# Optimization experiments

Measured on AMD Instinct MI355X. Metric: run time of the kernel, lower is better.

The kernel has to match this reference:

```python
import jax, jax.numpy as jnp
import numpy as np

N_NODES = 100000
N_EDGES = 1600000
IN_FEATS = 128
HIDDEN = 64
OUT_FEATS = 64
N_LABELS = 8


def setup_inputs() -> dict:
    key = jax.random.key(0)
    ks = jax.random.split(key, 10)
    glorot = lambda k, fi, fo: jax.random.normal(k, (fi, fo), jnp.float32) * jnp.sqrt(2.0 / (fi + fo))
    return {
        "features": jax.random.normal(ks[0], (N_NODES, IN_FEATS), jnp.float32),
        "edge_src": jax.random.randint(ks[1], (N_EDGES,), 0, N_NODES, jnp.int32),
        "edge_dst": jax.random.randint(ks[2], (N_EDGES,), 0, N_NODES, jnp.int32),
        "edge_types": jax.random.randint(ks[3], (N_EDGES,), 0, 4, jnp.int32),
        "W1": glorot(ks[4], IN_FEATS, HIDDEN),
        "b1": jnp.zeros((HIDDEN,), jnp.float32),
        "W2": glorot(ks[5], HIDDEN, OUT_FEATS),
        "b2": jnp.zeros((OUT_FEATS,), jnp.float32),
        "Wp": glorot(ks[6], OUT_FEATS, N_LABELS),
        "bp": jnp.zeros((N_LABELS,), jnp.float32),
    }


def _degree_norms(edge_src, edge_dst, n_nodes):
    ones = jnp.ones(edge_src.shape[0], jnp.float32)
    deg_out = jax.ops.segment_sum(ones, edge_src, num_segments=n_nodes)
    deg_in = jax.ops.segment_sum(ones, edge_dst, num_segments=n_nodes)
    # DGL clamps degrees to min 1 before pow(-0.5)
    norm_src = jnp.maximum(deg_out, 1.0) ** -0.5  # [N]
    norm_dst = jnp.maximum(deg_in, 1.0) ** -0.5   # [N]
    return norm_src, norm_dst


def _graph_conv(x, W, b, edge_src, edge_dst, norm_src, norm_dst, n_nodes):
    # norm='both': scale src, dense transform first (mult_first), aggregate, scale dst
    h = (x * norm_src[:, None]) @ W            # [N, out]
    msg = h[edge_src]                          # [E, out] gather
    agg = jax.ops.segment_sum(msg, edge_dst, num_segments=n_nodes)  # [N, out] scatter-add
    return agg * norm_dst[:, None] + b


def reference(features, edge_src, edge_dst, edge_types, W1, b1, W2, b2, Wp, bp):
    n_nodes = features.shape[0]
    norm_src, norm_dst = _degree_norms(edge_src, edge_dst, n_nodes)
    x = jax.nn.relu(_graph_conv(features, W1, b1, edge_src, edge_dst, norm_src, norm_dst, n_nodes))
    # dropout is identity in eval mode
    x = jax.nn.relu(_graph_conv(x, W2, b2, edge_src, edge_dst, norm_src, norm_dst, n_nodes))
    logits = x @ Wp + bp                       # [N, n_labels]
    return jax.nn.softmax(logits, axis=1)
```

## Files before the change

### kernel.cpp

```cpp
#include <hip/hip_runtime.h>
#include <hip/hip_fp16.h>
#include <math.h>


#define NODES   100000
#define INF     128
#define HID     64
#define NLAB    8

#define SB      512
#define NSB     ((NODES + SB - 1) / SB)
#define NHALF   ((NODES + 255) / 256)
#define CAP1    9000
#define SCAP    9000
#define CAP2    4600
#define PCHUNK  8192
#define PEPT    (PCHUNK / 256)
#define SRCMASK 0x1FFFF
#define GSTRIDE 16

#define WCVT_ELEMS (64 * (INF + 8) + 64 * (HID + 8))
#define WCVT_WGS   ((WCVT_ELEMS + 255) / 256)

union H8 { int4 i4; __half2 h2[4]; };

typedef _Float16 half8 __attribute__((ext_vector_type(8)));
typedef float floatx4 __attribute__((ext_vector_type(4)));


__global__ void build1_kernel(const int* __restrict__ src, const int* __restrict__ dst,
                              int* __restrict__ gcur_d, int* __restrict__ gcur_s,
                              int* __restrict__ dreg, unsigned short* __restrict__ sreg,
                              int E, int partWGs,
                              const float* __restrict__ W1, const float* __restrict__ W2,
                              _Float16* __restrict__ wt1, _Float16* __restrict__ wt2) {
    __shared__ int hd[NSB], hs[NSB], bd[NSB], bs[NSB];
    const int tid = threadIdx.x;

    if (blockIdx.x >= partWGs) {
        const int N1 = 64 * (INF + 8);
        const int N2 = 64 * (HID + 8);
        int i = (blockIdx.x - partWGs) * 256 + tid;
        if (i < N1) {
            int n = i / (INF + 8), k = i % (INF + 8);
            wt1[i] = (k < INF) ? (_Float16)W1[k * 64 + n] : (_Float16)0.f;
        } else if (i < N1 + N2) {
            int j = i - N1;
            int n = j / (HID + 8), k = j % (HID + 8);
            wt2[j] = (k < HID) ? (_Float16)W2[k * 64 + n] : (_Float16)0.f;
        }
        return;
    }

    const int e0 = blockIdx.x * PCHUNK;

    for (int i = tid; i < NSB; i += 256) { hd[i] = 0; hs[i] = 0; }
    __syncthreads();

    int es[PEPT], ed[PEPT];
#pragma unroll
    for (int i = 0; i < PEPT; ++i) {
        int e = e0 + tid + i * 256;
        if (e < E) {
            es[i] = src[e]; ed[i] = dst[e];
            atomicAdd(&hd[ed[i] >> 9], 1);
            atomicAdd(&hs[es[i] >> 9], 1);
        } else es[i] = -1;
    }
    __syncthreads();

    for (int b = tid; b < NSB; b += 256) {
        int c = hd[b]; bd[b] = c ? atomicAdd(&gcur_d[b * GSTRIDE], c) : 0;
        c = hs[b];     bs[b] = c ? atomicAdd(&gcur_s[b * GSTRIDE], c) : 0;
    }
    __syncthreads();
    for (int b = tid; b < NSB; b += 256) { hd[b] = 0; hs[b] = 0; }
    __syncthreads();

#pragma unroll
    for (int i = 0; i < PEPT; ++i) {
        if (es[i] >= 0) {
            int s = es[i], d = ed[i];
            int kb = d >> 9;
            int pos = bd[kb] + atomicAdd(&hd[kb], 1);
            if (pos < CAP1) dreg[(size_t)kb * CAP1 + pos] = ((d & (SB - 1)) << 17) | s;
            int ks = s >> 9;
            int ps = bs[ks] + atomicAdd(&hs[ks], 1);
            if (ps < SCAP) sreg[(size_t)ks * SCAP + ps] = (unsigned short)(s & (SB - 1));
        }
    }
}


__global__ void shist_kernel(const unsigned short* __restrict__ sreg,
                             const int* __restrict__ gcur_s,
                             float* __restrict__ norm_s, int Nn) {
    __shared__ int hist[SB];
    const int tid = threadIdx.x;
    const int sb = blockIdx.x;
    for (int i = tid; i < SB; i += 256) hist[i] = 0;
    __syncthreads();
    const int cnt = min(gcur_s[sb * GSTRIDE], SCAP);
    const unsigned short* base = sreg + (size_t)sb * SCAP;
    for (int i = tid; i < cnt; i += 256) atomicAdd(&hist[base[i]], 1);
    __syncthreads();
    for (int t = tid; t < SB; t += 256) {
        int node = sb * SB + t;
        if (node < Nn) norm_s[node] = rsqrtf(fmaxf((float)hist[t], 1.0f));
    }
}


__global__ void build2_kernel(const int* __restrict__ dreg, const int* __restrict__ gcur_d,
                              int* __restrict__ csr, int* __restrict__ starts,
                              int* __restrict__ ends, float* __restrict__ norm_d,
                              const float* __restrict__ Xv, const float* __restrict__ norm,
                              const _Float16* __restrict__ Wt, __half* __restrict__ Hh,
                              int Nn) {
    __shared__ union SMem {
        struct CS { int hist[256]; int excl[256]; int cur[256]; int tot; int sorted[CAP2]; } c;
        _Float16 w[64 * (INF + 8)];
    } sm;
    const int tid = threadIdx.x;

    if (blockIdx.x < NHALF) {
        const int j = blockIdx.x;
        const int sb = j >> 1, half = j & 1;
        const int cnt = min(gcur_d[sb * GSTRIDE], CAP1);
        const int* reg = dreg + (size_t)sb * CAP1;

        sm.c.hist[tid] = 0;
        __syncthreads();

        for (int i = tid; i < cnt; i += 256) {
            int pe = reg[i];
            if (((pe >> 25) & 1) == half) atomicAdd(&sm.c.hist[(pe >> 17) & 255], 1);
        }
        __syncthreads();

        sm.c.excl[tid] = sm.c.hist[tid];
        __syncthreads();
        for (int off = 1; off < 256; off <<= 1) {
            int v = (tid >= off) ? sm.c.excl[tid - off] : 0;
            __syncthreads();
            sm.c.excl[tid] += v;
            __syncthreads();
        }
        int deg_n = sm.c.hist[tid];
        int st = sm.c.excl[tid] - deg_n;
        if (tid == 255) sm.c.tot = min(sm.c.excl[255], CAP2);
        int node = j * 256 + tid;
        if (node < Nn) {
            int gs = j * CAP2 + st;
            int dcl = min(deg_n, max(CAP2 - st, 0));
            starts[node] = gs;
            ends[node]   = gs + dcl;
            norm_d[node] = rsqrtf(fmaxf((float)deg_n, 1.0f));
        }
        sm.c.cur[tid] = st;
        __syncthreads();

        for (int i = tid; i < cnt; i += 256) {
            int pe = reg[i];
            if (((pe >> 25) & 1) == half) {
                int pos = atomicAdd(&sm.c.cur[(pe >> 17) & 255], 1);
                if (pos < CAP2) sm.c.sorted[pos] = pe & SRCMASK;
            }
        }
        __syncthreads();

        const int tot = sm.c.tot;
        for (int i = tid; i < tot; i += 256) csr[(size_t)j * CAP2 + i] = sm.c.sorted[i];
        return;
    }

    constexpr int K = INF;
    constexpr int KP = K + 8;
    const int bid = blockIdx.x - NHALF;

    constexpr int NI4 = 64 * KP * 2 / 16;
    for (int i = tid; i < NI4; i += 256)
        ((int4*)sm.w)[i] = ((const int4*)Wt)[i];
    __syncthreads();

    const int w = tid >> 6, lane = tid & 63;
    const int m16 = lane & 15, quad = lane >> 4;
    const int rowA = bid * 64 + w * 16 + m16;
    const int rowC = (rowA < Nn) ? rowA : (Nn - 1);

    floatx4 acc0 = {0.f, 0.f, 0.f, 0.f};
    floatx4 acc1 = acc0, acc2 = acc0, acc3 = acc0;

#pragma unroll
    for (int c = 0; c < K / 32; ++c) {
        const int k0 = c * 32 + quad * 8;
        const float* xrow = Xv + (size_t)rowC * K;
        float4 xa = *(const float4*)(xrow + k0);
        float4 xb = *(const float4*)(xrow + k0 + 4);
        half8 a;
        a[0] = (_Float16)xa.x; a[1] = (_Float16)xa.y;
        a[2] = (_Float16)xa.z; a[3] = (_Float16)xa.w;
        a[4] = (_Float16)xb.x; a[5] = (_Float16)xb.y;
        a[6] = (_Float16)xb.z; a[7] = (_Float16)xb.w;
        half8 b0 = *(const half8*)&sm.w[(0 * 16 + m16) * KP + k0];
        half8 b1 = *(const half8*)&sm.w[(1 * 16 + m16) * KP + k0];
        half8 b2 = *(const half8*)&sm.w[(2 * 16 + m16) * KP + k0];
        half8 b3 = *(const half8*)&sm.w[(3 * 16 + m16) * KP + k0];
        acc0 = __builtin_amdgcn_mfma_f32_16x16x32_f16(a, b0, acc0, 0, 0, 0);
        acc1 = __builtin_amdgcn_mfma_f32_16x16x32_f16(a, b1, acc1, 0, 0, 0);
        acc2 = __builtin_amdgcn_mfma_f32_16x16x32_f16(a, b2, acc2, 0, 0, 0);
        acc3 = __builtin_amdgcn_mfma_f32_16x16x32_f16(a, b3, acc3, 0, 0, 0);
    }

    const int rbase = bid * 64 + w * 16 + quad * 4;
    floatx4 accs[4] = {acc0, acc1, acc2, acc3};
#pragma unroll
    for (int i = 0; i < 4; ++i) {
        int grow = rbase + i;
        if (grow < Nn) {
            float nm = norm[grow];
            __half* o = Hh + (size_t)grow * 64 + m16;
#pragma unroll
            for (int t = 0; t < 4; ++t)
                o[16 * t] = (__half)(accs[t][i] * nm);
        }
    }
}


template <int K, bool IN16>
__global__ void gemm_mfma_kernel(const void* __restrict__ Xv, const float* __restrict__ norm,
                                 const _Float16* __restrict__ Wt, __half* __restrict__ Hh,
                                 int M) {
    constexpr int KP = K + 8;
    __shared__ _Float16 sWt[64 * KP];

    const int tid = threadIdx.x;
    constexpr int NI4 = 64 * KP * 2 / 16;
    for (int i = tid; i < NI4; i += 256)
        ((int4*)sWt)[i] = ((const int4*)Wt)[i];
    __syncthreads();

    const int w = tid >> 6, lane = tid & 63;
    const int m16 = lane & 15, quad = lane >> 4;
    const int rowA = blockIdx.x * 64 + w * 16 + m16;
    const int rowC = (rowA < M) ? rowA : (M - 1);

    floatx4 acc0 = {0.f, 0.f, 0.f, 0.f};
    floatx4 acc1 = acc0, acc2 = acc0, acc3 = acc0;

#pragma unroll
    for (int c = 0; c < K / 32; ++c) {
        const int k0 = c * 32 + quad * 8;
        half8 a;
        if constexpr (IN16) {
            const _Float16* xrow = (const _Float16*)Xv + (size_t)rowC * K;
            a = *(const half8*)(xrow + k0);
        } else {
            const float* xrow = (const float*)Xv + (size_t)rowC * K;
            float4 xa = *(const float4*)(xrow + k0);
            float4 xb = *(const float4*)(xrow + k0 + 4);
            a[0] = (_Float16)xa.x; a[1] = (_Float16)xa.y;
            a[2] = (_Float16)xa.z; a[3] = (_Float16)xa.w;
            a[4] = (_Float16)xb.x; a[5] = (_Float16)xb.y;
            a[6] = (_Float16)xb.z; a[7] = (_Float16)xb.w;
        }
        half8 b0 = *(const half8*)&sWt[(0 * 16 + m16) * KP + k0];
        half8 b1 = *(const half8*)&sWt[(1 * 16 + m16) * KP + k0];
        half8 b2 = *(const half8*)&sWt[(2 * 16 + m16) * KP + k0];
        half8 b3 = *(const half8*)&sWt[(3 * 16 + m16) * KP + k0];
        acc0 = __builtin_amdgcn_mfma_f32_16x16x32_f16(a, b0, acc0, 0, 0, 0);
        acc1 = __builtin_amdgcn_mfma_f32_16x16x32_f16(a, b1, acc1, 0, 0, 0);
        acc2 = __builtin_amdgcn_mfma_f32_16x16x32_f16(a, b2, acc2, 0, 0, 0);
        acc3 = __builtin_amdgcn_mfma_f32_16x16x32_f16(a, b3, acc3, 0, 0, 0);
    }

    const int rbase = blockIdx.x * 64 + w * 16 + quad * 4;
    floatx4 accs[4] = {acc0, acc1, acc2, acc3};
#pragma unroll
    for (int i = 0; i < 4; ++i) {
        int grow = rbase + i;
        if (grow < M) {
            float nm = norm[grow];
            __half* o = Hh + (size_t)grow * 64 + m16;
#pragma unroll
            for (int t = 0; t < 4; ++t)
                o[16 * t] = (__half)(accs[t][i] * nm);
        }
    }
}


template <bool PROJ>
__global__ void gather_kernel(const int* __restrict__ starts, const int* __restrict__ ends,
                              const int* __restrict__ csr, const __half* __restrict__ Hh,
                              const float* __restrict__ nd, const float* __restrict__ b,
                              __half* __restrict__ Xh, const float* __restrict__ Wp,
                              const float* __restrict__ bp, float* __restrict__ out,
                              int Nn) {
    __shared__ float sW[NLAB * 65];
    __shared__ float sb_[NLAB];
    const int tid = threadIdx.x;

    if constexpr (PROJ) {
        for (int i = tid; i < 64 * NLAB; i += 256) {
            int k = i >> 3, l = i & 7;
            sW[l * 65 + k] = Wp[i];
        }
        if (tid < NLAB) sb_[tid] = bp[tid];
        __syncthreads();
    }

    const int lane = tid & 63;
    const int half32 = (lane >> 5) & 1;
    const int l32 = lane & 31;
    const int g = l32 >> 3;
    const int c = lane & 7;

    int node = blockIdx.x * 8 + ((tid >> 6) << 1) + half32;
    const bool valid = node < Nn;
    const int nodeC = valid ? node : (Nn - 1);

    const int start = starts[nodeC];
    const int deg   = ends[nodeC] - start;
    const int dmax  = max(deg, __shfl_xor(deg, 32, 64));

    float acc[8] = {0.f, 0.f, 0.f, 0.f, 0.f, 0.f, 0.f, 0.f};

    for (int base = 0; base < dmax; base += 32) {
        int off = base + l32;
        int pe = (off < deg) ? csr[start + off] : 0;
        int ec  = min(deg - base, 32);
        int ecm = min(dmax - base, 32);
        int nkp = (ecm + 7) >> 3;

        for (int k = 0; k < nkp; ++k) {
            int j0 = g + 8 * k;
            int j1 = j0 + 4;
            int s0 = __shfl(pe, (lane & 32) + j0, 64);
            int s1 = __shfl(pe, (lane & 32) + j1, 64);
            H8 v0, v1;
            if (j0 < ec) v0.i4 = ((const int4*)(Hh + (size_t)s0 * 64))[c];
            else         v0.i4 = make_int4(0, 0, 0, 0);
            if (j1 < ec) v1.i4 = ((const int4*)(Hh + (size_t)s1 * 64))[c];
            else         v1.i4 = make_int4(0, 0, 0, 0);
#pragma unroll
            for (int t = 0; t < 4; ++t) {
                __half2 s = __hadd2(v0.h2[t], v1.h2[t]);
                float2 f = __half22float2(s);
                acc[2 * t]     += f.x;
                acc[2 * t + 1] += f.y;
            }
        }
    }

#pragma unroll
    for (int m = 8; m <= 16; m <<= 1) {
#pragma unroll
        for (int k = 0; k < 8; ++k)
            acc[k] += __shfl_xor(acc[k], m, 64);
    }

    if constexpr (!PROJ) {
        if (g == 0 && valid) {
            float nm = nd[node];
            float4 b0 = ((const float4*)b)[2 * c];
            float4 b1 = ((const float4*)b)[2 * c + 1];
            H8 o;
            o.h2[0] = __floats2half2_rn(fmaxf(fmaf(acc[0], nm, b0.x), 0.f),
                                        fmaxf(fmaf(acc[1], nm, b0.y), 0.f));
            o.h2[1] = __floats2half2_rn(fmaxf(fmaf(acc[2], nm, b0.z), 0.f),
                                        fmaxf(fmaf(acc[3], nm, b0.w), 0.f));
            o.h2[2] = __floats2half2_rn(fmaxf(fmaf(acc[4], nm, b1.x), 0.f),
                                        fmaxf(fmaf(acc[5], nm, b1.y), 0.f));
            o.h2[3] = __floats2half2_rn(fmaxf(fmaf(acc[6], nm, b1.z), 0.f),
                                        fmaxf(fmaf(acc[7], nm, b1.w), 0.f));
            ((int4*)(Xh + (size_t)node * 64))[c] = o.i4;
        }
    } else {
        float nm = nd[nodeC];
        float4 b0 = ((const float4*)b)[2 * c];
        float4 b1 = ((const float4*)b)[2 * c + 1];
        float xv[8];
        xv[0] = fmaxf(fmaf(acc[0], nm, b0.x), 0.f);
        xv[1] = fmaxf(fmaf(acc[1], nm, b0.y), 0.f);
        xv[2] = fmaxf(fmaf(acc[2], nm, b0.z), 0.f);
        xv[3] = fmaxf(fmaf(acc[3], nm, b0.w), 0.f);
        xv[4] = fmaxf(fmaf(acc[4], nm, b1.x), 0.f);
        xv[5] = fmaxf(fmaf(acc[5], nm, b1.y), 0.f);
        xv[6] = fmaxf(fmaf(acc[6], nm, b1.z), 0.f);
        xv[7] = fmaxf(fmaf(acc[7], nm, b1.w), 0.f);

        const int l0 = 2 * g, l1 = l0 + 1;
        float p0 = 0.f, p1 = 0.f;
#pragma unroll
        for (int j = 0; j < 8; ++j) {
            p0 = fmaf(xv[j], sW[l0 * 65 + 8 * c + j], p0);
            p1 = fmaf(xv[j], sW[l1 * 65 + 8 * c + j], p1);
        }
        p0 += __shfl_xor(p0, 1, 64); p1 += __shfl_xor(p1, 1, 64);
        p0 += __shfl_xor(p0, 2, 64); p1 += __shfl_xor(p1, 2, 64);
        p0 += __shfl_xor(p0, 4, 64); p1 += __shfl_xor(p1, 4, 64);
        p0 += sb_[l0];
        p1 += sb_[l1];
        float mx = fmaxf(p0, p1);
        mx = fmaxf(mx, __shfl_xor(mx, 8, 64));
        mx = fmaxf(mx, __shfl_xor(mx, 16, 64));
        float e0 = __expf(p0 - mx), e1 = __expf(p1 - mx);
        float s2 = e0 + e1;
        s2 += __shfl_xor(s2, 8, 64);
        s2 += __shfl_xor(s2, 16, 64);
        float inv = 1.0f / s2;
        if (c == 0 && valid) {
            float2 o = {e0 * inv, e1 * inv};
            *(float2*)(out + (size_t)node * NLAB + l0) = o;
        }
    }
}


extern "C" void kernel_launch(void* const* d_in, const int* in_sizes, int n_in,
                              void* d_out, int out_size, void* d_ws, size_t ws_size,
                              hipStream_t stream) {
    const float* features = (const float*)d_in[0];
    const int*   edge_src = (const int*)d_in[1];
    const int*   edge_dst = (const int*)d_in[2];
    const float* W1 = (const float*)d_in[4];
    const float* b1 = (const float*)d_in[5];
    const float* W2 = (const float*)d_in[6];
    const float* b2 = (const float*)d_in[7];
    const float* Wp = (const float*)d_in[8];
    const float* bp = (const float*)d_in[9];
    float* out = (float*)d_out;

    const int N = NODES;
    const int E = in_sizes[1];

    char* p = (char*)d_ws;
    int*   csr    = (int*)p;            p += sizeof(int) * (size_t)NHALF * CAP2;
    int*   starts = (int*)p;            p += sizeof(int) * N;
    int*   ends   = (int*)p;            p += sizeof(int) * N;
    float* norm_s = (float*)p;          p += sizeof(float) * N;
    float* norm_d = (float*)p;          p += sizeof(float) * N;
    int*   gcur_d = (int*)p;            p += sizeof(int) * NSB * GSTRIDE;
    int*   gcur_s = (int*)p;            p += sizeof(int) * NSB * GSTRIDE;
    p = (char*)(((size_t)p + 255) & ~(size_t)255);
    _Float16* wt1 = (_Float16*)p;       p += sizeof(_Float16) * 64 * (INF + 8);
    _Float16* wt2 = (_Float16*)p;       p += sizeof(_Float16) * 64 * (HID + 8);
    p = (char*)(((size_t)p + 255) & ~(size_t)255);
    __half* h     = (__half*)p;         p += sizeof(__half) * (size_t)N * 64;
    p = (char*)(((size_t)p + 255) & ~(size_t)255);
    __half* x     = (__half*)p;         p += sizeof(__half) * (size_t)N * 64;
    int*            dreg = (int*)x;
    unsigned short* sreg = (unsigned short*)((char*)x + sizeof(int) * (size_t)NSB * CAP1);

    hipMemsetAsync(gcur_d, 0, sizeof(int) * 2 * NSB * GSTRIDE, stream);

    const int partWGs = (E + PCHUNK - 1) / PCHUNK;
    build1_kernel<<<partWGs + WCVT_WGS, 256, 0, stream>>>(edge_src, edge_dst,
                                                          gcur_d, gcur_s, dreg, sreg,
                                                          E, partWGs, W1, W2, wt1, wt2);
    shist_kernel<<<NSB, 256, 0, stream>>>(sreg, gcur_s, norm_s, N);
    build2_kernel<<<NHALF + (N + 63) / 64, 256, 0, stream>>>(dreg, gcur_d, csr, starts,
                                                             ends, norm_d,
                                                             features, norm_s, wt1, h, N);

    gather_kernel<false><<<(N + 7) / 8, 256, 0, stream>>>(starts, ends, csr, h, norm_d,
                                                          b1, x, nullptr, nullptr,
                                                          nullptr, N);

    gemm_mfma_kernel<HID, true><<<(N + 63) / 64, 256, 0, stream>>>(x, norm_s, wt2, h, N);
    gather_kernel<true><<<(N + 7) / 8, 256, 0, stream>>>(starts, ends, csr, h, norm_d,
                                                         b2, nullptr, Wp, bp, out, N);
}
```

Measured before the change: 249.7 us.

## Bucket destination edges per 256-node half-block and use fma_mix accumulation

Destination edges are now partitioned directly into 256-node buckets instead of 512-node buckets. Each build2 workgroup therefore reads only its own edges, with no half-filter that discards about half of what it loads. The block prefix scan now uses wavefront shuffles instead of a multi-barrier shared-memory scan. The gather inner loop converts fp16 to fp32 and adds in one step with v_fma_mix instructions. The costs are double the number of global bucket counters and atomics in build1, and inline assembly tied to the target ISA.

```diff
diff --git a/kernel.cpp b/kernel.cpp
--- a/kernel.cpp
+++ b/kernel.cpp
@@ -11,9 +11,8 @@
 #define SB      512
 #define NSB     ((NODES + SB - 1) / SB)
 #define NHALF   ((NODES + 255) / 256)
-#define CAP1    9000
 #define SCAP    9000
-#define CAP2    4600
+#define CAPH    4600
 #define PCHUNK  8192
 #define PEPT    (PCHUNK / 256)
 #define SRCMASK 0x1FFFF
@@ -22,10 +21,17 @@
 #define WCVT_ELEMS (64 * (INF + 8) + 64 * (HID + 8))
 #define WCVT_WGS   ((WCVT_ELEMS + 255) / 256)
 
-union H8 { int4 i4; __half2 h2[4]; };
+union H8 { int4 i4; __half2 h2[4]; unsigned int u[4]; };
+union H2U { __half2 h; unsigned int u; };
 
 typedef _Float16 half8 __attribute__((ext_vector_type(8)));
 typedef float floatx4 __attribute__((ext_vector_type(4)));
+
+__device__ __forceinline__ void fma_mix2(float& a0, float& a1, unsigned int h2) {
+    asm("v_fma_mix_f32 %0, %2, 1.0, %0 op_sel_hi:[1,0,0]\n\t"
+        "v_fma_mix_f32 %1, %2, 1.0, %1 op_sel:[1,0,0] op_sel_hi:[1,0,0]"
+        : "+v"(a0), "+v"(a1) : "v"(h2));
+}
 
 
 __global__ void build1_kernel(const int* __restrict__ src, const int* __restrict__ dst,
@@ -34,7 +40,7 @@
                               int E, int partWGs,
                               const float* __restrict__ W1, const float* __restrict__ W2,
                               _Float16* __restrict__ wt1, _Float16* __restrict__ wt2) {
-    __shared__ int hd[NSB], hs[NSB], bd[NSB], bs[NSB];
+    __shared__ int hd[NHALF], bd[NHALF], hs[NSB], bs[NSB];
     const int tid = threadIdx.x;
 
     if (blockIdx.x >= partWGs) {
@@ -54,7 +60,8 @@
 
     const int e0 = blockIdx.x * PCHUNK;
 
-    for (int i = tid; i < NSB; i += 256) { hd[i] = 0; hs[i] = 0; }
+    for (int i = tid; i < NHALF; i += 256) { hd[i] = 0; }
+    for (int i = tid; i < NSB; i += 256) { hs[i] = 0; }
     __syncthreads();
 
     int es[PEPT], ed[PEPT];
@@ -63,27 +70,30 @@
         int e = e0 + tid + i * 256;
         if (e < E) {
             es[i] = src[e]; ed[i] = dst[e];
-            atomicAdd(&hd[ed[i] >> 9], 1);
+            atomicAdd(&hd[ed[i] >> 8], 1);
             atomicAdd(&hs[es[i] >> 9], 1);
         } else es[i] = -1;
     }
     __syncthreads();
 
+    for (int b = tid; b < NHALF; b += 256) {
+        int c = hd[b]; bd[b] = c ? atomicAdd(&gcur_d[b * GSTRIDE], c) : 0;
+    }
     for (int b = tid; b < NSB; b += 256) {
-        int c = hd[b]; bd[b] = c ? atomicAdd(&gcur_d[b * GSTRIDE], c) : 0;
-        c = hs[b];     bs[b] = c ? atomicAdd(&gcur_s[b * GSTRIDE], c) : 0;
-    }
-    __syncthreads();
-    for (int b = tid; b < NSB; b += 256) { hd[b] = 0; hs[b] = 0; }
+        int c = hs[b]; bs[b] = c ? atomicAdd(&gcur_s[b * GSTRIDE], c) : 0;
+    }
+    __syncthreads();
+    for (int b = tid; b < NHALF; b += 256) hd[b] = 0;
+    for (int b = tid; b < NSB; b += 256) hs[b] = 0;
     __syncthreads();
 
 #pragma unroll
     for (int i = 0; i < PEPT; ++i) {
         if (es[i] >= 0) {
             int s = es[i], d = ed[i];
-            int kb = d >> 9;
+            int kb = d >> 8;
             int pos = bd[kb] + atomicAdd(&hd[kb], 1);
-            if (pos < CAP1) dreg[(size_t)kb * CAP1 + pos] = ((d & (SB - 1)) << 17) | s;
+            if (pos < CAPH) dreg[(size_t)kb * CAPH + pos] = ((d & 255) << 17) | s;
             int ks = s >> 9;
             int ps = bs[ks] + atomicAdd(&hs[ks], 1);
             if (ps < SCAP) sreg[(size_t)ks * SCAP + ps] = (unsigned short)(s & (SB - 1));
@@ -118,41 +128,42 @@
                               const _Float16* __restrict__ Wt, __half* __restrict__ Hh,
                               int Nn) {
     __shared__ union SMem {
-        struct CS { int hist[256]; int excl[256]; int cur[256]; int tot; int sorted[CAP2]; } c;
+        struct CS { int hist[256]; int cur[256]; int wsum[4]; int sorted[CAPH]; } c;
         _Float16 w[64 * (INF + 8)];
     } sm;
     const int tid = threadIdx.x;
 
     if (blockIdx.x < NHALF) {
         const int j = blockIdx.x;
-        const int sb = j >> 1, half = j & 1;
-        const int cnt = min(gcur_d[sb * GSTRIDE], CAP1);
-        const int* reg = dreg + (size_t)sb * CAP1;
+        const int cnt = min(gcur_d[j * GSTRIDE], CAPH);
+        const int* reg = dreg + (size_t)j * CAPH;
 
         sm.c.hist[tid] = 0;
         __syncthreads();
 
-        for (int i = tid; i < cnt; i += 256) {
-            int pe = reg[i];
-            if (((pe >> 25) & 1) == half) atomicAdd(&sm.c.hist[(pe >> 17) & 255], 1);
-        }
-        __syncthreads();
-
-        sm.c.excl[tid] = sm.c.hist[tid];
-        __syncthreads();
-        for (int off = 1; off < 256; off <<= 1) {
-            int v = (tid >= off) ? sm.c.excl[tid - off] : 0;
-            __syncthreads();
-            sm.c.excl[tid] += v;
-            __syncthreads();
-        }
+        for (int i = tid; i < cnt; i += 256)
+            atomicAdd(&sm.c.hist[(reg[i] >> 17) & 255], 1);
+        __syncthreads();
+
+        const int lane = tid & 63, wid = tid >> 6;
         int deg_n = sm.c.hist[tid];
-        int st = sm.c.excl[tid] - deg_n;
-        if (tid == 255) sm.c.tot = min(sm.c.excl[255], CAP2);
+        int v = deg_n;
+#pragma unroll
+        for (int off = 1; off < 64; off <<= 1) {
+            int u = __shfl_up(v, off, 64);
+            if (lane >= off) v += u;
+        }
+        if (lane == 63) sm.c.wsum[wid] = v;
+        __syncthreads();
+        int wadd = 0;
+#pragma unroll
+        for (int q = 0; q < 3; ++q) wadd += (q < wid) ? sm.c.wsum[q] : 0;
+        int st = v + wadd - deg_n;
+
         int node = j * 256 + tid;
         if (node < Nn) {
-            int gs = j * CAP2 + st;
-            int dcl = min(deg_n, max(CAP2 - st, 0));
+            int gs = j * CAPH + st;
+            int dcl = min(deg_n, max(CAPH - st, 0));
             starts[node] = gs;
             ends[node]   = gs + dcl;
             norm_d[node] = rsqrtf(fmaxf((float)deg_n, 1.0f));
@@ -162,15 +173,12 @@
 
         for (int i = tid; i < cnt; i += 256) {
             int pe = reg[i];
-            if (((pe >> 25) & 1) == half) {
-                int pos = atomicAdd(&sm.c.cur[(pe >> 17) & 255], 1);
-                if (pos < CAP2) sm.c.sorted[pos] = pe & SRCMASK;
-            }
-        }
-        __syncthreads();
-
-        const int tot = sm.c.tot;
-        for (int i = tid; i < tot; i += 256) csr[(size_t)j * CAP2 + i] = sm.c.sorted[i];
+            int pos = atomicAdd(&sm.c.cur[(pe >> 17) & 255], 1);
+            if (pos < CAPH) sm.c.sorted[pos] = pe & SRCMASK;
+        }
+        __syncthreads();
+
+        for (int i = tid; i < cnt; i += 256) csr[(size_t)j * CAPH + i] = sm.c.sorted[i];
         return;
     }
 
@@ -346,10 +354,9 @@
             else         v1.i4 = make_int4(0, 0, 0, 0);
 #pragma unroll
             for (int t = 0; t < 4; ++t) {
-                __half2 s = __hadd2(v0.h2[t], v1.h2[t]);
-                float2 f = __half22float2(s);
-                acc[2 * t]     += f.x;
-                acc[2 * t + 1] += f.y;
+                H2U su;
+                su.h = __hadd2(v0.h2[t], v1.h2[t]);
+                fma_mix2(acc[2 * t], acc[2 * t + 1], su.u);
             }
         }
     }
@@ -437,12 +444,12 @@
     const int E = in_sizes[1];
 
     char* p = (char*)d_ws;
-    int*   csr    = (int*)p;            p += sizeof(int) * (size_t)NHALF * CAP2;
+    int*   csr    = (int*)p;            p += sizeof(int) * (size_t)NHALF * CAPH;
     int*   starts = (int*)p;            p += sizeof(int) * N;
     int*   ends   = (int*)p;            p += sizeof(int) * N;
     float* norm_s = (float*)p;          p += sizeof(float) * N;
     float* norm_d = (float*)p;          p += sizeof(float) * N;
-    int*   gcur_d = (int*)p;            p += sizeof(int) * NSB * GSTRIDE;
+    int*   gcur_d = (int*)p;            p += sizeof(int) * NHALF * GSTRIDE;
     int*   gcur_s = (int*)p;            p += sizeof(int) * NSB * GSTRIDE;
     p = (char*)(((size_t)p + 255) & ~(size_t)255);
     _Float16* wt1 = (_Float16*)p;       p += sizeof(_Float16) * 64 * (INF + 8);
@@ -452,9 +459,9 @@
     p = (char*)(((size_t)p + 255) & ~(size_t)255);
     __half* x     = (__half*)p;         p += sizeof(__half) * (size_t)N * 64;
     int*            dreg = (int*)x;
-    unsigned short* sreg = (unsigned short*)((char*)x + sizeof(int) * (size_t)NSB * CAP1);
-
-    hipMemsetAsync(gcur_d, 0, sizeof(int) * 2 * NSB * GSTRIDE, stream);
+    unsigned short* sreg = (unsigned short*)((char*)x + sizeof(int) * (size_t)NHALF * CAPH);
+
+    hipMemsetAsync(gcur_d, 0, sizeof(int) * (NHALF + NSB) * GSTRIDE, stream);
 
     const int partWGs = (E + PCHUNK - 1) / PCHUNK;
     build1_kernel<<<partWGs + WCVT_WGS, 256, 0, stream>>>(edge_src, edge_dst,
```

Measured after the change: 241.9 us. 3.1% less time.
